# Kernel tuning notes

Hardware: AMD Instinct MI355X
Metric: run time of the kernel (lower is better)

Reference implementation:

```python
import jax, jax.numpy as jnp
import numpy as np

B, N, DIM = 2, 2048, 512
HEADS, DIM_HEAD = 8, 64
TIME_DIM = 512
EPS = 1e-5
NEG = 1e6


def setup_inputs() -> dict:
    key = jax.random.key(0)
    ks = jax.random.split(key, 8)
    return {
        "x": jax.random.normal(ks[0], (B, N, DIM), jnp.float32),
        "time": jax.random.normal(ks[1], (B, 1, TIME_DIM), jnp.float32),
        "attn_bias": jax.random.normal(ks[2], (B, HEADS, N, N), jnp.float32) * 0.1,
        "seq_mask": jnp.ones((B, N), jnp.float32),
        "gamma": jnp.ones((DIM,), jnp.float32),
        "w_time": jax.random.normal(ks[3], (2 * DIM, TIME_DIM), jnp.float32) * 0.02,
        "b_time": jax.random.normal(ks[4], (2 * DIM,), jnp.float32) * 0.02,
        "w_q": jax.random.normal(ks[5], (HEADS * DIM_HEAD, DIM), jnp.float32) * 0.02,
        "w_kv": jax.random.normal(ks[6], (2 * HEADS * DIM_HEAD, DIM), jnp.float32) * 0.02,
        "w_out": jax.random.normal(ks[7], (DIM, HEADS * DIM_HEAD), jnp.float32) * 0.02,
    }


def reference(x, time, attn_bias, seq_mask, gamma, w_time, b_time, w_q, w_kv, w_out):
    # NOTE: context = x BEFORE norm/time-cond/mask (faithful to original ordering)
    context = x
    # LayerNorm (beta buffer is zeros)
    mu = jnp.mean(x, axis=-1, keepdims=True)
    var = jnp.mean(jnp.square(x - mu), axis=-1, keepdims=True)
    xn = (x - mu) * jax.lax.rsqrt(var + EPS) * gamma
    # FiLM time conditioning: SiLU -> Linear -> (scale, shift)
    t = jax.nn.silu(time) @ w_time.T + b_time            # [b,1,2*dim]
    sc, sh = jnp.split(t, 2, axis=-1)
    xn = xn * (sc + 1.0) + sh
    # sequence mask on queries' input
    xn = xn * seq_mask[..., None]
    # projections
    q = (xn @ w_q.T).reshape(B, N, HEADS, DIM_HEAD).transpose(0, 2, 1, 3)   # b h n d
    kv = context @ w_kv.T                                                    # [b,n,2*h*d]
    k, v = jnp.split(kv, 2, axis=-1)
    k = k.reshape(B, N, HEADS, DIM_HEAD).transpose(0, 2, 1, 3)
    v = v.reshape(B, N, HEADS, DIM_HEAD).transpose(0, 2, 1, 3)
    q = q * (DIM_HEAD ** -0.5)
    # attention scores with additive bias and pairwise seq mask
    sim = jnp.einsum('bhid,bhjd->bhij', q, k) + attn_bias
    pair_mask = seq_mask[:, None, :, None] * seq_mask[:, None, None, :]      # b 1 i j
    sim = sim - (1.0 - pair_mask) * NEG
    attn = jax.nn.softmax(sim, axis=-1)
    out = jnp.einsum('bhij,bhjd->bhid', attn, v)
    out = out.transpose(0, 2, 1, 3).reshape(B, N, HEADS * DIM_HEAD)
    out = out @ w_out.T
    out = out * seq_mask[..., None]
    return out
```

## Files before the change

kernel.cpp:

```cpp
#include <hip/hip_runtime.h>
#include <stdint.h>


using s16x8 = __attribute__((ext_vector_type(8))) short;
using f32x4 = __attribute__((ext_vector_type(4))) float;
using u16x4 = __attribute__((ext_vector_type(4))) unsigned short;
using u32x2 = __attribute__((ext_vector_type(2))) unsigned int;

#define EPSV 1e-5f
#define NEGV 1e6f
#define L2E  1.44269504088896341f
#define QSCL 0.18033688011112043f

__device__ __forceinline__ unsigned short f2bf(float f) {
    unsigned int u = __float_as_uint(f);
    u += 0x7FFFu + ((u >> 16) & 1u);
    return (unsigned short)(u >> 16);
}
__device__ __forceinline__ float bf2f(unsigned short s) {
    return __uint_as_float((unsigned int)s << 16);
}

__device__ __forceinline__ void gl_lds16(const void* g, void* l) {
    __builtin_amdgcn_global_load_lds((const __attribute__((address_space(1))) void*)g,
                                     (__attribute__((address_space(3))) void*)l, 16, 0, 0);
}

__device__ __forceinline__ f32x4 mfma_bf16(s16x8 a, s16x8 b, f32x4 c) {
    return __builtin_amdgcn_mfma_f32_16x16x32_bf16(a, b, c, 0, 0, 0);
}

__global__ void k_prep(const float* __restrict__ w_q, const float* __restrict__ w_kv,
                       const float* __restrict__ w_out,
                       unsigned short* __restrict__ wq, unsigned short* __restrict__ wkv,
                       unsigned short* __restrict__ wo_h, unsigned short* __restrict__ wo_l) {
    int idx = blockIdx.x * 256 + threadIdx.x;
    if (idx < 262144) {
        wq[idx] = f2bf(w_q[idx]);
    } else if (idx < 786432) {
        int i = idx - 262144;
        wkv[i] = f2bf(w_kv[i]);
    } else {
        int i = idx - 786432;
        float v = w_out[i];
        unsigned short h = f2bf(v);
        wo_h[i] = h;
        wo_l[i] = f2bf(v - bf2f(h));
    }
}

__global__ void k_time(const float* __restrict__ timev, const float* __restrict__ w_time,
                       const float* __restrict__ b_time, float* __restrict__ tc) {
    int wid = threadIdx.x >> 6, lane = threadIdx.x & 63;
    int b = blockIdx.x >> 8;
    int j = (blockIdx.x & 255) * 4 + wid;
    const float* tv = timev + b * 512;
    const float* wr = w_time + (size_t)j * 512;
    float acc = 0.f;
#pragma unroll
    for (int i = 0; i < 8; ++i) {
        int k = i * 64 + lane;
        float t = tv[k];
        float s = t / (1.f + __expf(-t));
        acc += s * wr[k];
    }
#pragma unroll
    for (int m = 32; m >= 1; m >>= 1) acc += __shfl_xor(acc, m);
    if (lane == 0) tc[b * 1024 + j] = acc + b_time[j];
}

__global__ void k_lnfilm(const float* __restrict__ x, const float* __restrict__ gamma,
                         const float* __restrict__ seq_mask, const float* __restrict__ tc,
                         unsigned short* __restrict__ xbf, unsigned short* __restrict__ xnbf) {
    int row = blockIdx.x;
    int b = row >> 11;
    int tid = threadIdx.x, wid = tid >> 6, lane = tid & 63;
    float2 xv = *(const float2*)(x + (size_t)row * 512 + tid * 2);
    float s = xv.x + xv.y;
    float sq = xv.x * xv.x + xv.y * xv.y;
#pragma unroll
    for (int m = 32; m >= 1; m >>= 1) { s += __shfl_xor(s, m); sq += __shfl_xor(sq, m); }
    __shared__ float red[8];
    if (lane == 0) { red[wid] = s; red[wid + 4] = sq; }
    __syncthreads();
    float ts = red[0] + red[1] + red[2] + red[3];
    float tq = red[4] + red[5] + red[6] + red[7];
    float mu = ts * (1.f / 512.f);
    float var = tq * (1.f / 512.f) - mu * mu;
    float rs = rsqrtf(var + EPSV);
    float qm = seq_mask[row];
    int j = tid * 2;
    const float* scb = tc + b * 1024;
    float o0 = ((xv.x - mu) * rs * gamma[j])     * (scb[j] + 1.f)     + scb[j + 512];
    float o1 = ((xv.y - mu) * rs * gamma[j + 1]) * (scb[j + 1] + 1.f) + scb[j + 513];
    size_t base = (size_t)row * 512 + j;
    xnbf[base]     = f2bf(o0 * qm);
    xnbf[base + 1] = f2bf(o1 * qm);
    xbf[base]      = f2bf(xv.x);
    xbf[base + 1]  = f2bf(xv.y);
}

template<int EPI>
__launch_bounds__(256)
__global__ void k_gemm(const unsigned short* __restrict__ A, const unsigned short* __restrict__ W,
                       unsigned short* __restrict__ o0, unsigned short* __restrict__ o1) {
    __shared__ unsigned short a_t[128 * 64];
    __shared__ unsigned short b_t[128 * 64];
    int tid = threadIdx.x, lane = tid & 63, wid = tid >> 6;
    int lc = lane & 15, lq = lane >> 4;
    int wr = wid >> 1, wc = wid & 1;
    int m0 = blockIdx.x * 128, n0 = blockIdx.y * 128;
    f32x4 acc[4][4];
#pragma unroll
    for (int i = 0; i < 4; ++i)
#pragma unroll
        for (int jn = 0; jn < 4; ++jn)
#pragma unroll
            for (int e = 0; e < 4; ++e) acc[i][jn][e] = 0.f;
    const unsigned short* Ab = A + (size_t)m0 * 512;
    const unsigned short* Wb = W + (size_t)n0 * 512;
    int wbase = wid * 64;
    for (int kt = 0; kt < 8; ++kt) {
        __syncthreads();
#pragma unroll
        for (int i = 0; i < 4; ++i) {
            int p = i * 256 + wbase + lane;
            int row = p >> 3, ls = (p & 7) ^ (row & 7);
            gl_lds16(Ab + (size_t)row * 512 + kt * 64 + ls * 8, a_t + (i * 256 + wbase) * 8);
            gl_lds16(Wb + (size_t)row * 512 + kt * 64 + ls * 8, b_t + (i * 256 + wbase) * 8);
        }
        __syncthreads();
        s16x8 af[4][2], bw[4][2];
        const char* ab = (const char*)a_t;
        const char* bb = (const char*)b_t;
#pragma unroll
        for (int mf = 0; mf < 4; ++mf) {
            int row = wr * 64 + mf * 16 + lc;
            int key = (row & 7) << 4;
            af[mf][0] = *(const s16x8*)(ab + row * 128 + ((lq * 16) ^ key));
            af[mf][1] = *(const s16x8*)(ab + row * 128 + ((64 + lq * 16) ^ key));
        }
#pragma unroll
        for (int nf = 0; nf < 4; ++nf) {
            int row = wc * 64 + nf * 16 + lc;
            int key = (row & 7) << 4;
            bw[nf][0] = *(const s16x8*)(bb + row * 128 + ((lq * 16) ^ key));
            bw[nf][1] = *(const s16x8*)(bb + row * 128 + ((64 + lq * 16) ^ key));
        }
#pragma unroll
        for (int mf = 0; mf < 4; ++mf)
#pragma unroll
            for (int nf = 0; nf < 4; ++nf) {
                acc[mf][nf] = mfma_bf16(af[mf][0], bw[nf][0], acc[mf][nf]);
                acc[mf][nf] = mfma_bf16(af[mf][1], bw[nf][1], acc[mf][nf]);
            }
    }
#pragma unroll
    for (int mf = 0; mf < 4; ++mf)
#pragma unroll
        for (int nf = 0; nf < 4; ++nf) {
            int grow0 = m0 + wr * 64 + mf * 16 + lq * 4;
            int gcol = n0 + wc * 64 + nf * 16 + lc;
            int b = grow0 >> 11, nb = grow0 & 2047;
            if (EPI == 0) {
                int h = gcol >> 6, d = gcol & 63;
#pragma unroll
                for (int r = 0; r < 4; ++r)
                    o0[((size_t)((b * 8 + h) * 2048 + nb + r)) * 64 + d] =
                        f2bf(acc[mf][nf][r] * QSCL);
            } else if (gcol < 512) {
                int h = gcol >> 6, d = gcol & 63;
#pragma unroll
                for (int r = 0; r < 4; ++r)
                    o0[((size_t)((b * 8 + h) * 2048 + nb + r)) * 64 + d] = f2bf(acc[mf][nf][r]);
            } else {
                int jj = gcol & 511;
                int h = jj >> 6, d = jj & 63;
                u16x4 vv;
#pragma unroll
                for (int r = 0; r < 4; ++r) vv[r] = f2bf(acc[mf][nf][r]);
                *(u16x4*)(o1 + ((size_t)((b * 8 + h) * 64 + d)) * 2048 + nb) = vv;
            }
        }
}

__launch_bounds__(256)
__global__ void k_attn(const unsigned short* __restrict__ qg, const unsigned short* __restrict__ kg,
                       const unsigned short* __restrict__ vt, const float* __restrict__ bias,
                       const float* __restrict__ seq_mask,
                       unsigned short* __restrict__ ah, unsigned short* __restrict__ al) {
    __shared__ unsigned short k_ring[2][64 * 64];
    __shared__ unsigned short v_ring[2][64 * 64];
    __shared__ __align__(16) char b_ring[2][16384];
    __shared__ __align__(16) char scr[4][2048];

    int tid = threadIdx.x, lane = tid & 63, w = tid >> 6;
    int lc = lane & 15, lq = lane >> 4;

    int lin = blockIdx.x;
    int vid = (lin & 7) * 64 + (lin >> 3);
    int bh = vid >> 5;
    int q0 = (vid & 31) * 64 + w * 16;
    int b = bh >> 3, h = bh & 7;

    const unsigned short* qbase = qg + ((size_t)bh * 2048 + q0) * 64;
    s16x8 aq0 = *(const s16x8*)(qbase + lc * 64 + lq * 8);
    s16x8 aq1 = *(const s16x8*)(qbase + lc * 64 + 32 + lq * 8);

    const unsigned short* kb = kg + (size_t)bh * 2048 * 64;
    const unsigned short* vt0 = vt + (size_t)bh * 64 * 2048;
    const float* bqb = bias + ((size_t)bh * 2048 + q0) * 2048;
    const float* sk = seq_mask + b * 2048;
    const float NEG2 = NEGV * L2E;
    float qm_ = seq_mask[b * 2048 + q0 + lc];

    char* pw = &scr[w][0];
    int swz = (lc & 7) << 4;
    int brow = lane >> 4, bchk = lane & 15;

    float mst = -1e30f, lst = 0.f;
    f32x4 acc[4];
#pragma unroll
    for (int df = 0; df < 4; ++df)
#pragma unroll
        for (int e = 0; e < 4; ++e) acc[df][e] = 0.f;

    auto issue_k = [&](int tile, int slot) {
#pragma unroll
        for (int i = 0; i < 2; ++i) {
            int off = w * 2048 + i * 1024 + lane * 16;
            int row = off >> 7;
            int cc = ((off >> 4) & 7) ^ (row & 7);
            gl_lds16(kb + ((size_t)tile * 64 + row) * 64 + cc * 8,
                     (char*)k_ring[slot] + w * 2048 + i * 1024);
        }
    };
    auto issue_vt = [&](int tile, int slot) {
#pragma unroll
        for (int i = 0; i < 2; ++i) {
            int off = w * 2048 + i * 1024 + lane * 16;
            int row = off >> 7;
            int cc = ((off >> 4) & 7) ^ (row & 7);
            gl_lds16(vt0 + (size_t)row * 2048 + tile * 64 + cc * 8,
                     (char*)v_ring[slot] + w * 2048 + i * 1024);
        }
    };
    auto issue_b = [&](int tile, int slot) {
#pragma unroll
        for (int i = 0; i < 4; ++i) {
            int row = i * 4 + brow;
            int kc = bchk ^ (row & 7);
            gl_lds16(bqb + (size_t)row * 2048 + tile * 64 + kc * 4,
                     (char*)b_ring[slot] + w * 4096 + i * 1024);
        }
    };

    issue_k(0, 0);
    issue_vt(0, 0);
    issue_b(0, 0);
    __builtin_amdgcn_sched_barrier(0);
    asm volatile("s_waitcnt vmcnt(0)");
    __builtin_amdgcn_s_barrier();
    __builtin_amdgcn_sched_barrier(0);

    auto iter = [&](int kt, int par) {
        const int slot_nxt = par ^ 1;

        f32x4 km[4];
#pragma unroll
        for (int nf = 0; nf < 4; ++nf)
            km[nf] = *(const f32x4*)(sk + kt * 64 + nf * 16 + lq * 4);
        __builtin_amdgcn_sched_barrier(0);

        {
            int tk = (kt + 1 < 32) ? kt + 1 : 31;
            issue_k(tk, slot_nxt);
            issue_vt(tk, slot_nxt);
            __builtin_amdgcn_sched_barrier(0);
            issue_b(tk, slot_nxt);
        }
        __builtin_amdgcn_sched_barrier(0);

        const char* klds = (const char*)k_ring[par];
        f32x4 sv[4];
        __builtin_amdgcn_s_setprio(1);
#pragma unroll
        for (int nf = 0; nf < 4; ++nf) {
            int row = nf * 16 + lc;
            s16x8 b0 = *(const s16x8*)(klds + row * 128 + ((lq * 16) ^ swz));
            s16x8 b1 = *(const s16x8*)(klds + row * 128 + ((64 + lq * 16) ^ swz));
            f32x4 z;
            z[0] = 0.f; z[1] = 0.f; z[2] = 0.f; z[3] = 0.f;
            z = mfma_bf16(b0, aq0, z);
            z = mfma_bf16(b1, aq1, z);
            sv[nf] = z;
        }
        __builtin_amdgcn_s_setprio(0);

        __builtin_amdgcn_sched_barrier(0);
        asm volatile("s_waitcnt vmcnt(8)");
        __builtin_amdgcn_sched_barrier(0);
        const char* bws = (const char*)b_ring[par] + w * 4096;
        f32x4 bv[4];
#pragma unroll
        for (int nf = 0; nf < 4; ++nf)
            bv[nf] = *(const f32x4*)(bws + lc * 256 + ((((nf << 2) + lq) ^ (lc & 7)) << 4));

#pragma unroll
        for (int nf = 0; nf < 4; ++nf) {
#pragma unroll
            for (int e = 0; e < 4; ++e) {
                float pen = __builtin_fmaf(km[nf][e], qm_, -1.0f) * NEG2;
                sv[nf][e] = __builtin_fmaf(bv[nf][e], L2E, sv[nf][e]) + pen;
            }
        }

        f32x4 m4 = sv[0];
#pragma unroll
        for (int nf = 1; nf < 4; ++nf)
#pragma unroll
            for (int e = 0; e < 4; ++e) m4[e] = fmaxf(m4[e], sv[nf][e]);
        float mx = fmaxf(fmaxf(m4[0], m4[1]), fmaxf(m4[2], m4[3]));
        mx = fmaxf(mx, __shfl_xor(mx, 16));
        mx = fmaxf(mx, __shfl_xor(mx, 32));
        if (!__all(mx <= mst + 11.54f)) {
            float mn = fmaxf(mst, mx);
            float scl = __builtin_amdgcn_exp2f(mst - mn);
            lst *= scl;
#pragma unroll
            for (int df = 0; df < 4; ++df)
#pragma unroll
                for (int e = 0; e < 4; ++e) acc[df][e] *= scl;
            mst = mn;
        }
        float rsum = 0.f;
#pragma unroll
        for (int nf = 0; nf < 4; ++nf) {
            f32x4 p;
#pragma unroll
            for (int e = 0; e < 4; ++e) {
                p[e] = __builtin_amdgcn_exp2f(sv[nf][e] - mst);
                rsum += p[e];
            }
            unsigned int pk01, pk23;
            asm("v_cvt_pk_bf16_f32 %0, %1, %2" : "=v"(pk01) : "v"(p[0]), "v"(p[1]));
            asm("v_cvt_pk_bf16_f32 %0, %1, %2" : "=v"(pk23) : "v"(p[2]), "v"(p[3]));
            u32x2 pkv;
            pkv[0] = pk01; pkv[1] = pk23;
            *(u32x2*)(pw + lc * 128 + ((nf * 32 + lq * 8) ^ swz)) = pkv;
        }
        rsum += __shfl_xor(rsum, 16);
        rsum += __shfl_xor(rsum, 32);
        lst += rsum;

        __builtin_amdgcn_sched_barrier(0);
        asm volatile("s_waitcnt lgkmcnt(0)");
        __builtin_amdgcn_sched_barrier(0);

        s16x8 ap0 = *(const s16x8*)(pw + lc * 128 + ((lq * 16) ^ swz));
        s16x8 ap1 = *(const s16x8*)(pw + lc * 128 + ((64 + lq * 16) ^ swz));
        const char* vlds = (const char*)v_ring[par];
        __builtin_amdgcn_s_setprio(1);
#pragma unroll
        for (int df = 0; df < 4; ++df) {
            int row = df * 16 + lc;
            int key = (row & 7) << 4;
            s16x8 av0 = *(const s16x8*)(vlds + row * 128 + ((lq * 16) ^ key));
            s16x8 av1 = *(const s16x8*)(vlds + row * 128 + ((64 + lq * 16) ^ key));
            acc[df] = mfma_bf16(av0, ap0, acc[df]);
            acc[df] = mfma_bf16(av1, ap1, acc[df]);
        }
        __builtin_amdgcn_s_setprio(0);

        __builtin_amdgcn_sched_barrier(0);
        asm volatile("s_waitcnt vmcnt(4) lgkmcnt(0)");
        __builtin_amdgcn_s_barrier();
        __builtin_amdgcn_sched_barrier(0);
    };

    for (int t = 0; t < 16; ++t) {
        iter(2 * t,     0);
        iter(2 * t + 1, 1);
    }
    asm volatile("s_waitcnt vmcnt(0)");

    float inv = 1.f / lst;
    size_t rowb = ((size_t)(b * 2048 + q0 + lc)) * 512 + h * 64;
#pragma unroll
    for (int df = 0; df < 4; ++df) {
        u16x4 hi, lo;
#pragma unroll
        for (int r = 0; r < 4; ++r) {
            float o = acc[df][r] * inv;
            unsigned short hb = f2bf(o);
            hi[r] = hb;
            lo[r] = f2bf(o - bf2f(hb));
        }
        *(u16x4*)(ah + rowb + df * 16 + lq * 4) = hi;
        *(u16x4*)(al + rowb + df * 16 + lq * 4) = lo;
    }
}

__launch_bounds__(256)
__global__ void k_gemm_out(const unsigned short* __restrict__ Ah, const unsigned short* __restrict__ Al,
                           const unsigned short* __restrict__ Wh, const unsigned short* __restrict__ Wl,
                           const float* __restrict__ seq_mask, float* __restrict__ out) {
    __shared__ unsigned short ah_t[128 * 32], al_t[128 * 32], bh_t[128 * 32], bl_t[128 * 32];
    int tid = threadIdx.x, lane = tid & 63, wid = tid >> 6;
    int lc = lane & 15, lq = lane >> 4;
    int wr = wid >> 1, wc = wid & 1;
    int m0 = blockIdx.x * 128, n0 = blockIdx.y * 128;
    f32x4 acc[4][4];
#pragma unroll
    for (int i = 0; i < 4; ++i)
#pragma unroll
        for (int jn = 0; jn < 4; ++jn)
#pragma unroll
            for (int e = 0; e < 4; ++e) acc[i][jn][e] = 0.f;
    int wbase = wid * 64;
    for (int kt = 0; kt < 16; ++kt) {
        __syncthreads();
#pragma unroll
        for (int i = 0; i < 2; ++i) {
            int p = i * 256 + wbase + lane;
            int row = p >> 2, ls = (p & 3) ^ (row & 3);
            size_t asrc = (size_t)(m0 + row) * 512 + kt * 32 + ls * 8;
            size_t bsrc = (size_t)(n0 + row) * 512 + kt * 32 + ls * 8;
            int dst = (i * 256 + wbase) * 8;
            gl_lds16(Ah + asrc, ah_t + dst);
            gl_lds16(Al + asrc, al_t + dst);
            gl_lds16(Wh + bsrc, bh_t + dst);
            gl_lds16(Wl + bsrc, bl_t + dst);
        }
        __syncthreads();
        s16x8 fah[4], fal[4], fbh[4], fbl[4];
#pragma unroll
        for (int mf = 0; mf < 4; ++mf) {
            int row = wr * 64 + mf * 16 + lc;
            int off = row * 64 + ((lq * 16) ^ ((row & 3) << 4));
            fah[mf] = *(const s16x8*)((const char*)ah_t + off);
            fal[mf] = *(const s16x8*)((const char*)al_t + off);
        }
#pragma unroll
        for (int nf = 0; nf < 4; ++nf) {
            int row = wc * 64 + nf * 16 + lc;
            int off = row * 64 + ((lq * 16) ^ ((row & 3) << 4));
            fbh[nf] = *(const s16x8*)((const char*)bh_t + off);
            fbl[nf] = *(const s16x8*)((const char*)bl_t + off);
        }
#pragma unroll
        for (int mf = 0; mf < 4; ++mf)
#pragma unroll
            for (int nf = 0; nf < 4; ++nf) {
                acc[mf][nf] = mfma_bf16(fah[mf], fbh[nf], acc[mf][nf]);
                acc[mf][nf] = mfma_bf16(fah[mf], fbl[nf], acc[mf][nf]);
                acc[mf][nf] = mfma_bf16(fal[mf], fbh[nf], acc[mf][nf]);
            }
    }
#pragma unroll
    for (int mf = 0; mf < 4; ++mf)
#pragma unroll
        for (int nf = 0; nf < 4; ++nf)
#pragma unroll
            for (int r = 0; r < 4; ++r) {
                int grow = m0 + wr * 64 + mf * 16 + lq * 4 + r;
                int gcol = n0 + wc * 64 + nf * 16 + lc;
                out[(size_t)grow * 512 + gcol] = acc[mf][nf][r] * seq_mask[grow];
            }
}

extern "C" void kernel_launch(void* const* d_in, const int* in_sizes, int n_in,
                              void* d_out, int out_size, void* d_ws, size_t ws_size,
                              hipStream_t stream) {
    const float* x         = (const float*)d_in[0];
    const float* timev     = (const float*)d_in[1];
    const float* attn_bias = (const float*)d_in[2];
    const float* seq_mask  = (const float*)d_in[3];
    const float* gamma     = (const float*)d_in[4];
    const float* w_time    = (const float*)d_in[5];
    const float* b_time    = (const float*)d_in[6];
    const float* w_q       = (const float*)d_in[7];
    const float* w_kv      = (const float*)d_in[8];
    const float* w_out     = (const float*)d_in[9];
    float* out = (float*)d_out;

    char* ws = (char*)d_ws;
    size_t off = 0;
    auto alloc = [&](size_t bytes) {
        char* p = ws + off;
        off += (bytes + 255) & ~(size_t)255;
        return p;
    };
    float*          tc   = (float*)alloc(2048 * 4);
    unsigned short* wq   = (unsigned short*)alloc(262144 * 2);
    unsigned short* wkv  = (unsigned short*)alloc(524288 * 2);
    unsigned short* wo_h = (unsigned short*)alloc(262144 * 2);
    unsigned short* wo_l = (unsigned short*)alloc(262144 * 2);
    unsigned short* xbf  = (unsigned short*)alloc(2097152 * 2);
    unsigned short* xnbf = (unsigned short*)alloc(2097152 * 2);
    unsigned short* qb   = (unsigned short*)alloc(2097152 * 2);
    unsigned short* kb   = (unsigned short*)alloc(2097152 * 2);
    unsigned short* vtb  = (unsigned short*)alloc(2097152 * 2);
    unsigned short* ahh  = (unsigned short*)alloc(2097152 * 2);
    unsigned short* all_ = (unsigned short*)alloc(2097152 * 2);

    k_prep<<<4096, 256, 0, stream>>>(w_q, w_kv, w_out, wq, wkv, wo_h, wo_l);
    k_time<<<512, 256, 0, stream>>>(timev, w_time, b_time, tc);
    k_lnfilm<<<4096, 256, 0, stream>>>(x, gamma, seq_mask, tc, xbf, xnbf);
    k_gemm<0><<<dim3(32, 4), 256, 0, stream>>>(xnbf, wq, qb, nullptr);
    k_gemm<1><<<dim3(32, 8), 256, 0, stream>>>(xbf, wkv, kb, vtb);
    k_attn<<<512, 256, 0, stream>>>(qb, kb, vtb, attn_bias, seq_mask, ahh, all_);
    k_gemm_out<<<dim3(32, 4), 256, 0, stream>>>(ahh, all_, wo_h, wo_l, seq_mask, out);
}
```

Before: 142.0 us.

## Triple-buffer bias tiles with two-ahead prefetch and reuse bias slot for P

Bias tiles now use a three-slot LDS ring prefetched two key tiles ahead, so the mid-iteration wait on the bias load is removed and the end-of-iteration vmcnt is relaxed. The per-wave P scratch buffer is dropped and P is written into the already-consumed bias slot, and the key-mask loads are also prefetched one tile ahead into double-buffered registers. This hides the large fp32 bias stream's latency behind more compute. The cost is extra LDS for the third bias slot, more registers, and a dependence on the wait counts being exactly right.

```diff
diff --git a/kernel.cpp b/kernel.cpp
--- a/kernel.cpp
+++ b/kernel.cpp
@@ -191,8 +191,7 @@
                        unsigned short* __restrict__ ah, unsigned short* __restrict__ al) {
     __shared__ unsigned short k_ring[2][64 * 64];
     __shared__ unsigned short v_ring[2][64 * 64];
-    __shared__ __align__(16) char b_ring[2][16384];
-    __shared__ __align__(16) char scr[4][2048];
+    __shared__ __align__(16) char b_ring[3][16384];
 
     int tid = threadIdx.x, lane = tid & 63, w = tid >> 6;
     int lc = lane & 15, lq = lane >> 4;
@@ -214,7 +213,6 @@
     const float NEG2 = NEGV * L2E;
     float qm_ = seq_mask[b * 2048 + q0 + lc];
 
-    char* pw = &scr[w][0];
     int swz = (lc & 7) << 4;
     int brow = lane >> 4, bchk = lane & 15;
 
@@ -246,42 +244,47 @@
         }
     };
     auto issue_b = [&](int tile, int slot) {
+        char* base = b_ring[slot] + w * 4096;
 #pragma unroll
         for (int i = 0; i < 4; ++i) {
             int row = i * 4 + brow;
             int kc = bchk ^ (row & 7);
-            gl_lds16(bqb + (size_t)row * 2048 + tile * 64 + kc * 4,
-                     (char*)b_ring[slot] + w * 4096 + i * 1024);
+            gl_lds16(bqb + (size_t)row * 2048 + tile * 64 + kc * 4, base + i * 1024);
         }
     };
+
+    f32x4 kmA[4], kmB[4];
 
     issue_k(0, 0);
     issue_vt(0, 0);
     issue_b(0, 0);
+    issue_b(1, 1);
+    __builtin_amdgcn_sched_barrier(0);
+#pragma unroll
+    for (int nf = 0; nf < 4; ++nf)
+        kmA[nf] = *(const f32x4*)(sk + nf * 16 + lq * 4);
     __builtin_amdgcn_sched_barrier(0);
     asm volatile("s_waitcnt vmcnt(0)");
     __builtin_amdgcn_s_barrier();
     __builtin_amdgcn_sched_barrier(0);
 
-    auto iter = [&](int kt, int par) {
-        const int slot_nxt = par ^ 1;
-
-        f32x4 km[4];
+    auto iter = [&](int kt, int bs, f32x4 (&kmc)[4], f32x4 (&kmn)[4]) {
+        const int kvp = kt & 1;
+        int bs2 = bs + 2; if (bs2 >= 3) bs2 -= 3;
+        int tk1 = (kt + 1 < 32) ? kt + 1 : 31;
+        int tk2 = (kt + 2 < 32) ? kt + 2 : 31;
+
+        issue_k(tk1, kvp ^ 1);
+        issue_vt(tk1, kvp ^ 1);
+        __builtin_amdgcn_sched_barrier(0);
 #pragma unroll
         for (int nf = 0; nf < 4; ++nf)
-            km[nf] = *(const f32x4*)(sk + kt * 64 + nf * 16 + lq * 4);
-        __builtin_amdgcn_sched_barrier(0);
-
-        {
-            int tk = (kt + 1 < 32) ? kt + 1 : 31;
-            issue_k(tk, slot_nxt);
-            issue_vt(tk, slot_nxt);
-            __builtin_amdgcn_sched_barrier(0);
-            issue_b(tk, slot_nxt);
-        }
-        __builtin_amdgcn_sched_barrier(0);
-
-        const char* klds = (const char*)k_ring[par];
+            kmn[nf] = *(const f32x4*)(sk + tk1 * 64 + nf * 16 + lq * 4);
+        __builtin_amdgcn_sched_barrier(0);
+        issue_b(tk2, bs2);
+        __builtin_amdgcn_sched_barrier(0);
+
+        const char* klds = (const char*)k_ring[kvp];
         f32x4 sv[4];
         __builtin_amdgcn_s_setprio(1);
 #pragma unroll
@@ -297,10 +300,7 @@
         }
         __builtin_amdgcn_s_setprio(0);
 
-        __builtin_amdgcn_sched_barrier(0);
-        asm volatile("s_waitcnt vmcnt(8)");
-        __builtin_amdgcn_sched_barrier(0);
-        const char* bws = (const char*)b_ring[par] + w * 4096;
+        const char* bws = (const char*)b_ring[bs] + w * 4096;
         f32x4 bv[4];
 #pragma unroll
         for (int nf = 0; nf < 4; ++nf)
@@ -310,11 +310,12 @@
         for (int nf = 0; nf < 4; ++nf) {
 #pragma unroll
             for (int e = 0; e < 4; ++e) {
-                float pen = __builtin_fmaf(km[nf][e], qm_, -1.0f) * NEG2;
+                float pen = __builtin_fmaf(kmc[nf][e], qm_, -1.0f) * NEG2;
                 sv[nf][e] = __builtin_fmaf(bv[nf][e], L2E, sv[nf][e]) + pen;
             }
         }
 
+        char* pw = b_ring[bs] + w * 4096;
         f32x4 m4 = sv[0];
 #pragma unroll
         for (int nf = 1; nf < 4; ++nf)
@@ -359,7 +360,7 @@
 
         s16x8 ap0 = *(const s16x8*)(pw + lc * 128 + ((lq * 16) ^ swz));
         s16x8 ap1 = *(const s16x8*)(pw + lc * 128 + ((64 + lq * 16) ^ swz));
-        const char* vlds = (const char*)v_ring[par];
+        const char* vlds = (const char*)v_ring[kvp];
         __builtin_amdgcn_s_setprio(1);
 #pragma unroll
         for (int df = 0; df < 4; ++df) {
@@ -373,14 +374,17 @@
         __builtin_amdgcn_s_setprio(0);
 
         __builtin_amdgcn_sched_barrier(0);
-        asm volatile("s_waitcnt vmcnt(4) lgkmcnt(0)");
+        asm volatile("s_waitcnt vmcnt(8) lgkmcnt(0)");
         __builtin_amdgcn_s_barrier();
         __builtin_amdgcn_sched_barrier(0);
     };
 
-    for (int t = 0; t < 16; ++t) {
-        iter(2 * t,     0);
-        iter(2 * t + 1, 1);
+    int bs = 0;
+    for (int kt = 0; kt < 32; kt += 2) {
+        iter(kt, bs, kmA, kmB);
+        bs = (bs + 1 < 3) ? bs + 1 : 0;
+        iter(kt + 1, bs, kmB, kmA);
+        bs = (bs + 1 < 3) ? bs + 1 : 0;
     }
     asm volatile("s_waitcnt vmcnt(0)");
 
```

Measured after the change: 143.8 us. About the same (+1.3%).
